# Kernel optimization log

Measured on AMD Instinct MI355X. Metric: run time of the kernel, lower is better.

## Reference

```python
import jax, jax.numpy as jnp
import numpy as np

N, E, F, H = 50000, 500000, 128, 128   # nodes, edges, in-features, hidden
L, R, B = 3, 8, 30                     # layers, relations, bases
G, C = 16, 8                           # graphs in batch, classes
EPS = 1e-5


def setup_inputs() -> dict:
    key = jax.random.key(0)
    ks = jax.random.split(key, 16)
    x = jax.random.normal(ks[0], (N, F), jnp.float32)
    edge_index = jax.random.randint(ks[1], (2, E), 0, N)
    edge_attr = jax.random.randint(ks[2], (E,), 0, R)
    batch = jnp.sort(jax.random.randint(ks[3], (N,), 0, G))
    # RGCN params (all layers share shapes since F == H)
    basis = jax.random.normal(ks[4], (L, B, H, H), jnp.float32) * 0.05
    comp = jax.random.normal(ks[5], (L, R, B), jnp.float32) * 0.2
    root = jax.random.normal(ks[6], (L, H, H), jnp.float32) * 0.05
    bias = jnp.zeros((L, H), jnp.float32)
    # BatchNorm (eval mode: running stats)
    bn1_gamma = jnp.ones((F,), jnp.float32)
    bn1_beta = jnp.zeros((F,), jnp.float32)
    bn1_mean = jax.random.normal(ks[7], (F,), jnp.float32) * 0.1
    bn1_var = jax.random.uniform(ks[8], (F,), jnp.float32, 0.5, 1.5)
    bn2_gamma = jnp.ones((H,), jnp.float32)
    bn2_beta = jnp.zeros((H,), jnp.float32)
    bn2_mean = jax.random.normal(ks[9], (H,), jnp.float32) * 0.1
    bn2_var = jax.random.uniform(ks[10], (H,), jnp.float32, 0.5, 1.5)
    fc1_w = jax.random.normal(ks[11], (H, H), jnp.float32) * 0.05
    fc1_b = jnp.zeros((H,), jnp.float32)
    fc2_w = jax.random.normal(ks[12], (H, C), jnp.float32) * 0.05
    fc2_b = jnp.zeros((C,), jnp.float32)
    return dict(x=x, edge_index=edge_index, edge_attr=edge_attr, batch=batch,
                bn1_gamma=bn1_gamma, bn1_beta=bn1_beta, bn1_mean=bn1_mean, bn1_var=bn1_var,
                basis=basis, comp=comp, root=root, bias=bias,
                bn2_gamma=bn2_gamma, bn2_beta=bn2_beta, bn2_mean=bn2_mean, bn2_var=bn2_var,
                fc1_w=fc1_w, fc1_b=fc1_b, fc2_w=fc2_w, fc2_b=fc2_b)


def _bn(x, gamma, beta, mean, var):
    return (x - mean) * jax.lax.rsqrt(var + EPS) * gamma + beta


def _rgcn_layer(x, basis_l, comp_l, root_l, bias_l, src, dst, edge_attr):
    # root transform + bias
    out = x @ root_l + bias_l
    # relation-wise basis-decomposed message passing, mean-aggregated per relation
    for r in range(R):
        W_r = jnp.einsum('b,bio->io', comp_l[r], basis_l)  # [H, H]
        xw = x @ W_r                                       # [N, H]
        mask = (edge_attr == r).astype(x.dtype)            # [E]
        msg = xw[src] * mask[:, None]                      # gather + mask
        agg = jax.ops.segment_sum(msg, dst, num_segments=N)
        deg = jax.ops.segment_sum(mask, dst, num_segments=N)
        out = out + agg / jnp.maximum(deg, 1.0)[:, None]
    return out


def reference(x, edge_index, edge_attr, batch,
              bn1_gamma, bn1_beta, bn1_mean, bn1_var,
              basis, comp, root, bias,
              bn2_gamma, bn2_beta, bn2_mean, bn2_var,
              fc1_w, fc1_b, fc2_w, fc2_b):
    src, dst = edge_index[0], edge_index[1]
    h = _bn(x, bn1_gamma, bn1_beta, bn1_mean, bn1_var)
    for l in range(L):
        h = jax.nn.relu(_rgcn_layer(h, basis[l], comp[l], root[l], bias[l], src, dst, edge_attr))
        # dropout is identity in eval mode
    # global mean pool per graph
    sums = jax.ops.segment_sum(h, batch, num_segments=G)            # [G, H]
    counts = jax.ops.segment_sum(jnp.ones((N,), h.dtype), batch, num_segments=G)
    g = sums / jnp.maximum(counts, 1.0)[:, None]
    g = _bn(g, bn2_gamma, bn2_beta, bn2_mean, bn2_var)
    # temporal_type == 'mean'
    v = jax.nn.relu(g.mean(axis=0))                                 # [H]
    v = jax.nn.relu(v @ fc1_w + fc1_b)
    logits = v @ fc2_w + fc2_b                                      # [C]
    return jax.nn.log_softmax(logits, axis=-1)
```

## Files before the change

kernel.cpp:

```cpp
#include <hip/hip_runtime.h>
#include <hip/hip_bf16.h>

#define NN 50000
#define NE 500000
#define HID 128
#define LAYERS 3
#define RELS 8
#define BASES 30
#define GRAPHS 16
#define CLASSES 8
#define EPSV 1e-5f
#define NOUT (HID * (RELS + 1))
#define NSEG (NN * RELS)
#define SCAN_CHUNK 1024
#define SCAN_NBLK2 ((NSEG + SCAN_CHUNK - 1) / SCAN_CHUNK)
#define PCHUNK 128
#define DTILE 64
#define NDBLK ((NN + DTILE - 1) / DTILE)
#define ECAP 28

typedef __attribute__((ext_vector_type(8))) short short8;
typedef __attribute__((ext_vector_type(4))) float f32x4;

__device__ __forceinline__ float bf2f(unsigned short u) {
    union { unsigned int i; float f; } x; x.i = ((unsigned int)u) << 16; return x.f;
}
__device__ __forceinline__ unsigned short f2bf(float f) {
    __hip_bfloat16 b = __float2bfloat16(f);
    return *(unsigned short*)&b;
}
__device__ __forceinline__ float ubf_lo(unsigned w) {
    union { unsigned i; float f; } t; t.i = w << 16; return t.f;
}
__device__ __forceinline__ float ubf_hi(unsigned w) {
    union { unsigned i; float f; } t; t.i = w & 0xFFFF0000u; return t.f;
}
__device__ __forceinline__ int permf(int f) {
    return (f & 64) | ((f & 15) << 2) | ((f >> 4) & 3);
}
__device__ __forceinline__ int ipermf(int q) {
    return (q & 64) | ((q & 3) << 4) | ((q >> 2) & 15);
}
__device__ __forceinline__ void gload16(const void* g, void* l) {
    __builtin_amdgcn_global_load_lds(
        (const __attribute__((address_space(1))) unsigned int*)g,
        (__attribute__((address_space(3))) unsigned int*)l, 16, 0, 0);
}

__global__ __launch_bounds__(256) void build_wcat(const float* __restrict__ basis,
                                                  const float* __restrict__ comp,
                                                  const float* __restrict__ root,
                                                  unsigned short* __restrict__ wT) {
    int bid = blockIdx.x;
    int l = bid >> 6;
    int k0 = (bid & 63) << 1;
    __shared__ float cl[RELS * BASES];
    int tid = threadIdx.x;
    if (tid < RELS * BASES) cl[tid] = comp[l * RELS * BASES + tid];
    __syncthreads();
    int j = tid & 127;
    int k = k0 + (tid >> 7);
    int pk = permf(k);
    const float* bp = basis + ((size_t)l * BASES * HID + k) * HID + j;
    float acc[RELS];
#pragma unroll
    for (int r = 0; r < RELS; ++r) acc[r] = 0.f;
    for (int b = 0; b < BASES; ++b) {
        float v = bp[(size_t)b * HID * HID];
#pragma unroll
        for (int r = 0; r < RELS; ++r) acc[r] += cl[r * BASES + b] * v;
    }
    unsigned short* wl = wT + (size_t)l * NOUT * HID;
#pragma unroll
    for (int r = 0; r < RELS; ++r)
        wl[(size_t)((1 + r) * HID + j) * HID + pk] = f2bf(acc[r]);
    wl[(size_t)j * HID + pk] = f2bf(root[((size_t)l * HID + k) * HID + j]);
}

__global__ void bn1_kernel(const float* __restrict__ x, const float* __restrict__ gamma,
                           const float* __restrict__ beta, const float* __restrict__ mean,
                           const float* __restrict__ var, unsigned short* __restrict__ habf) {
    int idx = blockIdx.x * blockDim.x + threadIdx.x;
    if (idx >= NN * HID) return;
    int q = idx & (HID - 1);
    int n = idx >> 7;
    int f = ipermf(q);
    habf[idx] = f2bf((x[(n << 7) + f] - mean[f]) * rsqrtf(var[f] + EPSV) * gamma[f] + beta[f]);
}

__global__ void deg_kernel(const int* __restrict__ ei, const int* __restrict__ ea,
                           float* __restrict__ deg) {
    int e = blockIdx.x * blockDim.x + threadIdx.x;
    if (e >= NE) return;
    int dst = ei[NE + e];
    atomicAdd(&deg[(size_t)dst * RELS + ea[e]], 1.0f);
}

__global__ __launch_bounds__(256) void scan_partial(float* __restrict__ deg,
                                                    int* __restrict__ rowptr,
                                                    int* __restrict__ bsum) {
    __shared__ int ssc[256];
    int t = threadIdx.x;
    int base = blockIdx.x * SCAN_CHUNK + t * 4;
    int v[4];
#pragma unroll
    for (int j = 0; j < 4; ++j) {
        int seg = base + j;
        if (seg < NSEG) {
            float d = deg[seg];
            v[j] = (int)(d + 0.5f);
            deg[seg] = 1.0f / fmaxf(d, 1.0f);
        } else v[j] = 0;
    }
    int tsum = v[0] + v[1] + v[2] + v[3];
    ssc[t] = tsum;
    __syncthreads();
    for (int ofs = 1; ofs < 256; ofs <<= 1) {
        int add = (t >= ofs) ? ssc[t - ofs] : 0;
        __syncthreads();
        ssc[t] += add;
        __syncthreads();
    }
    int excl = ssc[t] - tsum;
    int e = 0;
#pragma unroll
    for (int j = 0; j < 4; ++j) {
        if (base + j < NSEG) rowptr[base + j] = excl + e;
        e += v[j];
    }
    if (t == 255) bsum[blockIdx.x] = ssc[255];
}

__global__ __launch_bounds__(512) void scan_bsum(int* __restrict__ bsum) {
    __shared__ int s[512];
    int t = threadIdx.x;
    int v = (t < SCAN_NBLK2) ? bsum[t] : 0;
    s[t] = v;
    __syncthreads();
    for (int o = 1; o < 512; o <<= 1) {
        int a = (t >= o) ? s[t - o] : 0;
        __syncthreads();
        s[t] += a;
        __syncthreads();
    }
    if (t < SCAN_NBLK2) bsum[t] = s[t] - v;
}

__global__ __launch_bounds__(256) void scan_add(int* __restrict__ rowptr,
                                                const int* __restrict__ bsum) {
    int i = blockIdx.x * blockDim.x + threadIdx.x;
    if (i < NSEG) rowptr[i] += bsum[i >> 10];
    if (i == 0) rowptr[NSEG] = NE;
}

__global__ void fill_kernel(const int* __restrict__ ei, const int* __restrict__ ea,
                            const int* __restrict__ rowptr,
                            int* __restrict__ fillcnt, int* __restrict__ epk) {
    int e = blockIdx.x * blockDim.x + threadIdx.x;
    if (e >= NE) return;
    int src = ei[e];
    int seg = ei[NE + e] * RELS + ea[e];
    int pos = atomicAdd(&fillcnt[seg], 1);
    epk[rowptr[seg] + pos] = src;
}

__global__ __launch_bounds__(256) void rgcn_layer(const unsigned short* __restrict__ hin,
                                                  const unsigned short* __restrict__ wTl,
                                                  const float* __restrict__ bias,
                                                  const int* __restrict__ rp2,
                                                  const int* __restrict__ epk2,
                                                  const float* __restrict__ invdeg,
                                                  unsigned short* __restrict__ hout) {
    __shared__ __align__(16) unsigned short As[DTILE * HID];
    __shared__ __align__(16) unsigned short Bs[128 * HID];
    __shared__ unsigned short bnd_l[DTILE * 9];
    __shared__ unsigned short src_l[DTILE * ECAP];
    __shared__ int base_l[DTILE];
    int row0 = blockIdx.x * DTILE;
    int tid = threadIdx.x;
    int wave = tid >> 6, lane = tid & 63;
    int quad = lane >> 4, l16 = lane & 15;
    int wn = wave * 32;
    int ld = tid >> 2, tq = tid & 3;
    int dst = row0 + ld;
    bool ok = dst < NN;

    f32x4 acc[4][2];
#pragma unroll
    for (int i = 0; i < 4; ++i)
#pragma unroll
        for (int j = 0; j < 2; ++j) acc[i][j] = (f32x4){0.f, 0.f, 0.f, 0.f};

    auto mfma_panel = [&]() {
#pragma unroll
        for (int kc = 0; kc < 4; ++kc) {
            int ca = ((kc * 4 + quad) ^ (l16 & 7)) << 3;
            short8 a[4], b[2];
#pragma unroll
            for (int i = 0; i < 4; ++i) a[i] = *(const short8*)&As[(i * 16 + l16) * HID + ca];
#pragma unroll
            for (int j = 0; j < 2; ++j) b[j] = *(const short8*)&Bs[(wn + j * 16 + l16) * HID + ca];
#pragma unroll
            for (int i = 0; i < 4; ++i)
#pragma unroll
                for (int j = 0; j < 2; ++j)
                    acc[i][j] = __builtin_amdgcn_mfma_f32_16x16x32_bf16(a[i], b[j], acc[i][j], 0, 0, 0);
        }
    };

    {
        int base = ok ? rp2[dst * RELS] : 0;
        int endt = ok ? rp2[dst * RELS + 8] : 0;
        int b0 = ok ? rp2[dst * RELS + tq] : 0;
        int b1 = ok ? rp2[dst * RELS + 4 + tq] : 0;
        bnd_l[ld * 9 + tq] = (unsigned short)(b0 - base);
        bnd_l[ld * 9 + 4 + tq] = (unsigned short)(b1 - base);
        if (tq == 0) {
            bnd_l[ld * 9 + 8] = (unsigned short)(endt - base);
            base_l[ld] = base;
        }
        int degt = endt - base;
        int lim = degt < ECAP ? degt : ECAP;
        for (int e = tq; e < lim; e += 4)
            src_l[ld * ECAP + e] = (unsigned short)epk2[base + e];
    }

#pragma unroll
    for (int q = 0; q < 4; ++q) {
        int rb = (wave << 4) + (q << 2);
        int r = rb + (lane >> 4), c = lane & 15;
        int ga = row0 + r; if (ga > NN - 1) ga = NN - 1;
        gload16(hin + (size_t)ga * HID + ((c ^ (r & 7)) << 3), &As[rb * HID]);
    }
#pragma unroll
    for (int q = 0; q < 8; ++q) {
        int rb = (wave << 5) + (q << 2);
        int r = rb + (lane >> 4), c = lane & 15;
        gload16(wTl + (size_t)r * HID + ((c ^ (r & 7)) << 3), &Bs[rb * HID]);
    }
    __syncthreads();
    mfma_panel();

    for (int p = 1; p <= RELS; ++p) {
        float ga[32];
#pragma unroll
        for (int i2 = 0; i2 < 32; ++i2) ga[i2] = 0.f;
        float s = 0.f;
        if (ok) {
            int seg = dst * RELS + (p - 1);
            s = invdeg[seg];
            int bl = bnd_l[ld * 9 + (p - 1)];
            int el = bnd_l[ld * 9 + p];
            int e = bl;
            for (; e + 2 <= el; e += 2) {
                int s0 = (e < ECAP) ? (int)src_l[ld * ECAP + e] : epk2[base_l[ld] + e];
                int s1 = (e + 1 < ECAP) ? (int)src_l[ld * ECAP + e + 1] : epk2[base_l[ld] + e + 1];
                const uint4* ra = (const uint4*)(hin + (size_t)s0 * HID + (tq << 5));
                const uint4* rb = (const uint4*)(hin + (size_t)s1 * HID + (tq << 5));
                uint4 a0 = ra[0], a1 = ra[1], a2 = ra[2], a3 = ra[3];
                uint4 b0 = rb[0], b1 = rb[1], b2 = rb[2], b3 = rb[3];
#pragma unroll
                for (int q4 = 0; q4 < 4; ++q4) {
                    uint4 u = (q4 == 0) ? a0 : (q4 == 1) ? a1 : (q4 == 2) ? a2 : a3;
                    uint4 v = (q4 == 0) ? b0 : (q4 == 1) ? b1 : (q4 == 2) ? b2 : b3;
                    ga[q4 * 8 + 0] += ubf_lo(u.x) + ubf_lo(v.x); ga[q4 * 8 + 1] += ubf_hi(u.x) + ubf_hi(v.x);
                    ga[q4 * 8 + 2] += ubf_lo(u.y) + ubf_lo(v.y); ga[q4 * 8 + 3] += ubf_hi(u.y) + ubf_hi(v.y);
                    ga[q4 * 8 + 4] += ubf_lo(u.z) + ubf_lo(v.z); ga[q4 * 8 + 5] += ubf_hi(u.z) + ubf_hi(v.z);
                    ga[q4 * 8 + 6] += ubf_lo(u.w) + ubf_lo(v.w); ga[q4 * 8 + 7] += ubf_hi(u.w) + ubf_hi(v.w);
                }
            }
            if (e < el) {
                int s0 = (e < ECAP) ? (int)src_l[ld * ECAP + e] : epk2[base_l[ld] + e];
                const uint4* ra = (const uint4*)(hin + (size_t)s0 * HID + (tq << 5));
                uint4 a0 = ra[0], a1 = ra[1], a2 = ra[2], a3 = ra[3];
#pragma unroll
                for (int q4 = 0; q4 < 4; ++q4) {
                    uint4 u = (q4 == 0) ? a0 : (q4 == 1) ? a1 : (q4 == 2) ? a2 : a3;
                    ga[q4 * 8 + 0] += ubf_lo(u.x); ga[q4 * 8 + 1] += ubf_hi(u.x);
                    ga[q4 * 8 + 2] += ubf_lo(u.y); ga[q4 * 8 + 3] += ubf_hi(u.y);
                    ga[q4 * 8 + 4] += ubf_lo(u.z); ga[q4 * 8 + 5] += ubf_hi(u.z);
                    ga[q4 * 8 + 6] += ubf_lo(u.w); ga[q4 * 8 + 7] += ubf_hi(u.w);
                }
            }
        }
        __syncthreads();
#pragma unroll
        for (int cc = 0; cc < 4; ++cc) {
            short8 v;
#pragma unroll
            for (int i2 = 0; i2 < 8; ++i2) v[i2] = (short)f2bf(ga[cc * 8 + i2] * s);
            int c = (tq << 2) + cc;
            *(short8*)&As[ld * HID + ((c ^ (ld & 7)) << 3)] = v;
        }
#pragma unroll
        for (int q = 0; q < 8; ++q) {
            int rb = (wave << 5) + (q << 2);
            int r = rb + (lane >> 4), c = lane & 15;
            gload16(wTl + (size_t)(p * 128 + r) * HID + ((c ^ (r & 7)) << 3), &Bs[rb * HID]);
        }
        __syncthreads();
        mfma_panel();
    }

    int pb = ((wave & 2) << 5) + (l16 << 2) + ((wave & 1) << 1);
    float b0 = bias[wn + l16], b1 = bias[wn + 16 + l16];
#pragma unroll
    for (int i = 0; i < 4; ++i)
#pragma unroll
        for (int reg = 0; reg < 4; ++reg) {
            int grow = row0 + i * 16 + quad * 4 + reg;
            if (grow >= NN) continue;
            unsigned u = (unsigned)f2bf(fmaxf(acc[i][0][reg] + b0, 0.f))
                       | ((unsigned)f2bf(fmaxf(acc[i][1][reg] + b1, 0.f)) << 16);
            *(unsigned*)(hout + (size_t)grow * HID + pb) = u;
        }
}

__global__ __launch_bounds__(256) void pool_kernel(const unsigned short* __restrict__ habf,
                                                   const int* __restrict__ batch,
                                                   float* __restrict__ psum,
                                                   float* __restrict__ pcnt) {
    int tid = threadIdx.x;
    int f = tid & 127;
    int sub = tid >> 7;
    int base = blockIdx.x * PCHUNK;
    float acc = 0.f, cnt = 0.f;
    int gcur = -1;
    for (int it = 0; it < PCHUNK / 2; ++it) {
        int node = base + it * 2 + sub;
        if (node >= NN) break;
        int g = batch[node];
        if (g != gcur) {
            if (gcur >= 0) {
                atomicAdd(&psum[gcur * HID + f], acc);
                if (f == 0) atomicAdd(&pcnt[gcur], cnt);
            }
            gcur = g; acc = 0.f; cnt = 0.f;
        }
        acc += bf2f(habf[(size_t)node * HID + f]);
        cnt += 1.f;
    }
    if (gcur >= 0) {
        atomicAdd(&psum[gcur * HID + f], acc);
        if (f == 0) atomicAdd(&pcnt[gcur], cnt);
    }
}

__global__ void head_kernel(const float* __restrict__ psum, const float* __restrict__ pcnt,
                            const float* __restrict__ g2, const float* __restrict__ b2,
                            const float* __restrict__ m2, const float* __restrict__ v2,
                            const float* __restrict__ fc1w, const float* __restrict__ fc1b,
                            const float* __restrict__ fc2w, const float* __restrict__ fc2b,
                            float* __restrict__ out) {
    __shared__ float v[HID];
    __shared__ float u[HID];
    __shared__ float lg[CLASSES];
    int j = threadIdx.x;
    int pj = permf(j);
    float acc = 0.f;
    for (int g = 0; g < GRAPHS; ++g) {
        float val = psum[g * HID + pj] / fmaxf(pcnt[g], 1.0f);
        val = (val - m2[j]) * rsqrtf(v2[j] + EPSV) * g2[j] + b2[j];
        acc += val;
    }
    v[j] = fmaxf(acc / (float)GRAPHS, 0.f);
    __syncthreads();
    float s = fc1b[j];
    for (int k = 0; k < HID; ++k) s += v[k] * fc1w[k * HID + j];
    u[j] = fmaxf(s, 0.f);
    __syncthreads();
    if (j < CLASSES) {
        float t = fc2b[j];
        for (int k = 0; k < HID; ++k) t += u[k] * fc2w[k * CLASSES + j];
        lg[j] = t;
    }
    __syncthreads();
    if (j < CLASSES) {
        float mx = lg[0];
        for (int c = 1; c < CLASSES; ++c) mx = fmaxf(mx, lg[c]);
        float se = 0.f;
        for (int c = 0; c < CLASSES; ++c) se += expf(lg[c] - mx);
        out[j] = lg[j] - mx - logf(se);
    }
}

extern "C" void kernel_launch(void* const* d_in, const int* in_sizes, int n_in,
                              void* d_out, int out_size, void* d_ws, size_t ws_size,
                              hipStream_t stream) {
    const float* x     = (const float*)d_in[0];
    const int*   ei    = (const int*)d_in[1];
    const int*   ea    = (const int*)d_in[2];
    const int*   batch = (const int*)d_in[3];
    const float* bn1g  = (const float*)d_in[4];
    const float* bn1b  = (const float*)d_in[5];
    const float* bn1m  = (const float*)d_in[6];
    const float* bn1v  = (const float*)d_in[7];
    const float* basis = (const float*)d_in[8];
    const float* comp  = (const float*)d_in[9];
    const float* root  = (const float*)d_in[10];
    const float* bias  = (const float*)d_in[11];
    const float* bn2g  = (const float*)d_in[12];
    const float* bn2b  = (const float*)d_in[13];
    const float* bn2m  = (const float*)d_in[14];
    const float* bn2v  = (const float*)d_in[15];
    const float* fc1w  = (const float*)d_in[16];
    const float* fc1b  = (const float*)d_in[17];
    const float* fc2w  = (const float*)d_in[18];
    const float* fc2b  = (const float*)d_in[19];

    float* ws = (float*)d_ws;
    size_t off = 0;
    unsigned short* wT  = (unsigned short*)(ws + off); off += (size_t)LAYERS * NOUT * HID / 2;
    unsigned short* hb0 = (unsigned short*)(ws + off); off += (size_t)NN * HID / 2;
    unsigned short* hb1 = (unsigned short*)(ws + off); off += (size_t)NN * HID / 2;
    float* deg    = ws + off; off += (size_t)NSEG;
    float* psum   = ws + off; off += (size_t)GRAPHS * HID + GRAPHS;
    float* pcnt   = psum + GRAPHS * HID;
    int* rowptr2  = (int*)(ws + off); off += (size_t)NSEG + 1;
    int* fillcnt2 = (int*)(ws + off); off += (size_t)NSEG;
    int* bsum     = (int*)(ws + off); off += (size_t)SCAN_NBLK2;
    int* epk2     = (int*)(ws + off); off += (size_t)NE;
    if (ws_size < off * sizeof(float)) return;

    hipMemsetAsync(psum, 0, (GRAPHS * HID + GRAPHS) * sizeof(float), stream);
    hipMemsetAsync(deg, 0, (size_t)NSEG * sizeof(float), stream);
    hipMemsetAsync(fillcnt2, 0, (size_t)NSEG * sizeof(int), stream);

    build_wcat<<<LAYERS * 64, 256, 0, stream>>>(basis, comp, root, wT);
    bn1_kernel<<<(NN * HID + 255) / 256, 256, 0, stream>>>(x, bn1g, bn1b, bn1m, bn1v, hb0);

    deg_kernel<<<(NE + 255) / 256, 256, 0, stream>>>(ei, ea, deg);
    scan_partial<<<SCAN_NBLK2, 256, 0, stream>>>(deg, rowptr2, bsum);
    scan_bsum<<<1, 512, 0, stream>>>(bsum);
    scan_add<<<(NSEG + 255) / 256, 256, 0, stream>>>(rowptr2, bsum);
    fill_kernel<<<(NE + 255) / 256, 256, 0, stream>>>(ei, ea, rowptr2, fillcnt2, epk2);

    const unsigned short* hin = hb0;
    unsigned short* hout = hb1;
    for (int l = 0; l < LAYERS; ++l) {
        rgcn_layer<<<NDBLK, 256, 0, stream>>>(hin, wT + (size_t)l * NOUT * HID,
                                              bias + (size_t)l * HID, rowptr2, epk2, deg, hout);
        const unsigned short* t = hin; hin = hout; hout = (unsigned short*)t;
    }

    pool_kernel<<<(NN + PCHUNK - 1) / PCHUNK, 256, 0, stream>>>(hin, batch, psum, pcnt);
    head_kernel<<<1, 128, 0, stream>>>(psum, pcnt, bn2g, bn2b, bn2m, bn2v,
                                       fc1w, fc1b, fc2w, fc2b, (float*)d_out);
}
```

Measured before the change: 468.3 us.

## Keep weight panel in registers and double-buffer A tile in LDS

Each wave now loads its slice of the per-relation weight panel straight from global memory into registers instead of staging all of B in shared memory. The A tile is double-buffered, which removes one __syncthreads per relation, and __launch_bounds__(256,4) is added. The smaller LDS footprint (about 32KB less per block) is meant to allow more resident blocks, improving occupancy and latency hiding for the gather. The cost is more vector registers for B and redundant global loads of the weights across blocks, though these should be served from cache.

```diff
diff --git a/kernel.cpp b/kernel.cpp
--- a/kernel.cpp
+++ b/kernel.cpp
@@ -164,15 +164,14 @@
     epk[rowptr[seg] + pos] = src;
 }
 
-__global__ __launch_bounds__(256) void rgcn_layer(const unsigned short* __restrict__ hin,
-                                                  const unsigned short* __restrict__ wTl,
-                                                  const float* __restrict__ bias,
-                                                  const int* __restrict__ rp2,
-                                                  const int* __restrict__ epk2,
-                                                  const float* __restrict__ invdeg,
-                                                  unsigned short* __restrict__ hout) {
-    __shared__ __align__(16) unsigned short As[DTILE * HID];
-    __shared__ __align__(16) unsigned short Bs[128 * HID];
+__global__ __launch_bounds__(256, 4) void rgcn_layer(const unsigned short* __restrict__ hin,
+                                                     const unsigned short* __restrict__ wTl,
+                                                     const float* __restrict__ bias,
+                                                     const int* __restrict__ rp2,
+                                                     const int* __restrict__ epk2,
+                                                     const float* __restrict__ invdeg,
+                                                     unsigned short* __restrict__ hout) {
+    __shared__ __align__(16) unsigned short As[2][DTILE * HID];
     __shared__ unsigned short bnd_l[DTILE * 9];
     __shared__ unsigned short src_l[DTILE * ECAP];
     __shared__ int base_l[DTILE];
@@ -191,20 +190,27 @@
 #pragma unroll
         for (int j = 0; j < 2; ++j) acc[i][j] = (f32x4){0.f, 0.f, 0.f, 0.f};
 
-    auto mfma_panel = [&]() {
+    uint4 b4[2][4];
+    auto loadB = [&](int p) {
+#pragma unroll
+        for (int j = 0; j < 2; ++j)
+#pragma unroll
+            for (int kc = 0; kc < 4; ++kc)
+                b4[j][kc] = *(const uint4*)(wTl + (size_t)(p * 128 + wn + j * 16 + l16) * HID
+                                            + ((kc * 4 + quad) << 3));
+    };
+    auto mfma_panel = [&](const unsigned short* Ab) {
 #pragma unroll
         for (int kc = 0; kc < 4; ++kc) {
             int ca = ((kc * 4 + quad) ^ (l16 & 7)) << 3;
-            short8 a[4], b[2];
-#pragma unroll
-            for (int i = 0; i < 4; ++i) a[i] = *(const short8*)&As[(i * 16 + l16) * HID + ca];
-#pragma unroll
-            for (int j = 0; j < 2; ++j) b[j] = *(const short8*)&Bs[(wn + j * 16 + l16) * HID + ca];
-#pragma unroll
-            for (int i = 0; i < 4; ++i)
-#pragma unroll
-                for (int j = 0; j < 2; ++j)
-                    acc[i][j] = __builtin_amdgcn_mfma_f32_16x16x32_bf16(a[i], b[j], acc[i][j], 0, 0, 0);
+            short8 a[4];
+#pragma unroll
+            for (int i = 0; i < 4; ++i) a[i] = *(const short8*)&Ab[(i * 16 + l16) * HID + ca];
+#pragma unroll
+            for (int i = 0; i < 4; ++i) {
+                acc[i][0] = __builtin_amdgcn_mfma_f32_16x16x32_bf16(a[i], *(const short8*)&b4[0][kc], acc[i][0], 0, 0, 0);
+                acc[i][1] = __builtin_amdgcn_mfma_f32_16x16x32_bf16(a[i], *(const short8*)&b4[1][kc], acc[i][1], 0, 0, 0);
+            }
         }
     };
 
@@ -230,18 +236,14 @@
         int rb = (wave << 4) + (q << 2);
         int r = rb + (lane >> 4), c = lane & 15;
         int ga = row0 + r; if (ga > NN - 1) ga = NN - 1;
-        gload16(hin + (size_t)ga * HID + ((c ^ (r & 7)) << 3), &As[rb * HID]);
-    }
-#pragma unroll
-    for (int q = 0; q < 8; ++q) {
-        int rb = (wave << 5) + (q << 2);
-        int r = rb + (lane >> 4), c = lane & 15;
-        gload16(wTl + (size_t)r * HID + ((c ^ (r & 7)) << 3), &Bs[rb * HID]);
-    }
-    __syncthreads();
-    mfma_panel();
+        gload16(hin + (size_t)ga * HID + ((c ^ (r & 7)) << 3), &As[0][rb * HID]);
+    }
+    loadB(0);
+    __syncthreads();
+    mfma_panel(As[0]);
 
     for (int p = 1; p <= RELS; ++p) {
+        loadB(p);
         float ga[32];
 #pragma unroll
         for (int i2 = 0; i2 < 32; ++i2) ga[i2] = 0.f;
@@ -283,23 +285,17 @@
                 }
             }
         }
-        __syncthreads();
+        unsigned short* Aw = &As[p & 1][0];
 #pragma unroll
         for (int cc = 0; cc < 4; ++cc) {
             short8 v;
 #pragma unroll
             for (int i2 = 0; i2 < 8; ++i2) v[i2] = (short)f2bf(ga[cc * 8 + i2] * s);
             int c = (tq << 2) + cc;
-            *(short8*)&As[ld * HID + ((c ^ (ld & 7)) << 3)] = v;
-        }
-#pragma unroll
-        for (int q = 0; q < 8; ++q) {
-            int rb = (wave << 5) + (q << 2);
-            int r = rb + (lane >> 4), c = lane & 15;
-            gload16(wTl + (size_t)(p * 128 + r) * HID + ((c ^ (r & 7)) << 3), &Bs[rb * HID]);
+            *(short8*)&Aw[ld * HID + ((c ^ (ld & 7)) << 3)] = v;
         }
         __syncthreads();
-        mfma_panel();
+        mfma_panel(&As[p & 1][0]);
     }
 
     int pb = ((wave & 2) << 5) + (l16 << 2) + ((wave & 1) << 1);
```

Measured after the change: 558.9 us. 1.19x slower.
